# Kernel optimization log

Hardware: AMD Instinct MI355X
Metric: run time of the kernel (lower is better)

Reference implementation:

```python
import jax, jax.numpy as jnp
import numpy as np
from jax import lax

EPS = 1e-5
BETA = 0.25  # commitment cost

def _conv(x, w, b):
    y = lax.conv_general_dilated(x, w, (1, 1), 'VALID',
                                 dimension_numbers=('NCHW', 'OIHW', 'NCHW'))
    return y + b[None, :, None, None]

def _maxpool2(x):
    return lax.reduce_window(x, -jnp.inf, lax.max, (1, 1, 2, 2), (1, 1, 2, 2), 'VALID')

def _bn(x, scale, bias):
    # training-mode batch norm over (N, H, W)
    mean = jnp.mean(x, axis=(0, 2, 3), keepdims=True)
    var = jnp.var(x, axis=(0, 2, 3), keepdims=True)
    xhat = (x - mean) * lax.rsqrt(var + EPS)
    return xhat * scale[None, :, None, None] + bias[None, :, None, None]

def _vq(z_nchw, codebook):
    # z: [B,32,4,4] -> vectors [B*16, 32]
    B, C, H, W = z_nchw.shape
    z = jnp.transpose(z_nchw, (0, 2, 3, 1)).reshape(-1, C)          # [N, D]
    # squared L2 distances to codebook [K, D]
    d = (jnp.sum(z * z, axis=1, keepdims=True)
         + jnp.sum(codebook * codebook, axis=1)
         - 2.0 * z @ codebook.T)                                    # [N, K]
    idx = jnp.argmin(d, axis=1)                                     # [N]
    q = codebook[idx]                                               # [N, D]
    sg = lax.stop_gradient
    vq_loss = jnp.mean((q - sg(z)) ** 2) + BETA * jnp.mean((sg(q) - z) ** 2)
    q_st = z + sg(q - z)                                            # straight-through
    recon = jnp.transpose(q_st.reshape(B, H, W, C), (0, 3, 1, 2))
    return recon, vq_loss

def setup_inputs() -> dict:
    key = jax.random.key(0)
    ks = jax.random.split(key, 12)
    f = lambda k, shape, s: (jax.random.normal(k, shape, jnp.float32) * s)
    inp = {
        'x': jax.random.normal(ks[0], (2048, 3, 32, 32), jnp.float32),
        'conv1_w': f(ks[1], (64, 3, 3, 3), 0.1), 'conv1_b': jnp.zeros((64,), jnp.float32),
        'bn1_scale': jnp.ones((64,), jnp.float32), 'bn1_bias': jnp.zeros((64,), jnp.float32),
        'conv2_w': f(ks[2], (32, 64, 3, 3), 0.05), 'conv2_b': jnp.zeros((32,), jnp.float32),
        'bn2_scale': jnp.ones((32,), jnp.float32), 'bn2_bias': jnp.zeros((32,), jnp.float32),
        'conv3_w': f(ks[3], (32, 32, 3, 3), 0.06), 'conv3_b': jnp.zeros((32,), jnp.float32),
        'bn3_scale': jnp.ones((32,), jnp.float32), 'bn3_bias': jnp.zeros((32,), jnp.float32),
        'codebook': f(ks[4], (100, 32), 0.5),
        'fc1_w': f(ks[5], (64, 512), 0.04), 'fc1_b': jnp.zeros((64,), jnp.float32),
        'fc2_w': f(ks[6], (10, 64), 0.12), 'fc2_b': jnp.zeros((10,), jnp.float32),
    }
    return inp

def reference(x, conv1_w, conv1_b, bn1_scale, bn1_bias,
              conv2_w, conv2_b, bn2_scale, bn2_bias,
              conv3_w, conv3_b, bn3_scale, bn3_bias,
              codebook, fc1_w, fc1_b, fc2_w, fc2_b):
    h = _bn(jax.nn.relu(_maxpool2(_conv(x, conv1_w, conv1_b))), bn1_scale, bn1_bias)
    h = _bn(jax.nn.relu(_maxpool2(_conv(h, conv2_w, conv2_b))), bn2_scale, bn2_bias)
    h = _bn(jax.nn.relu(_conv(h, conv3_w, conv3_b)), bn3_scale, bn3_bias)   # [B,32,4,4]
    recon, vq_loss = _vq(h, codebook)
    blended = 0.5 * recon + h
    flat = blended.reshape(-1, 4 * 4 * 32)
    z1 = jax.nn.relu(flat @ fc1_w.T + fc1_b)
    y = z1 @ fc2_w.T + fc2_b
    return recon, h, vq_loss, jax.nn.log_softmax(y, axis=1)
```

## Files before the change

kernel.cpp:

```cpp
#include <hip/hip_runtime.h>
#include <math.h>


#define CNT1 460800.0
#define CNT2 73728.0
#define CNT3 32768.0

__global__ void k0_w2t(const float* __restrict__ w2, float* __restrict__ w2t)
{
  const int idx = blockIdx.x * 256 + threadIdx.x;
  const int o = idx & 31, q = idx >> 5;
  const int r = q % 144, cc = q / 144;
  w2t[idx] = w2[o * 576 + cc * 144 + r];
}

__global__ __launch_bounds__(256) void k1_conv1_stats(
    const float* __restrict__ x, const float* __restrict__ w1,
    const float* __restrict__ b1, double* __restrict__ dstats,
    float* __restrict__ y1, int store_y1)
{
  __shared__ float img[3072];
  __shared__ float red[512];
  const int n = blockIdx.x, t = threadIdx.x;
  const float4* xin = (const float4*)(x + n * 3072);
  float4* img4 = (float4*)img;
  for (int i = t; i < 768; i += 256) img4[i] = xin[i];
  const int c = t >> 2, q = t & 3;
  float wr[27];
#pragma unroll
  for (int k = 0; k < 27; ++k) wr[k] = w1[c * 27 + k];
  const float bias = b1[c];
  __syncthreads();
  float s = 0.f, ss = 0.f;
  for (int p = q; p < 225; p += 4) {
    const int i = p / 15, j = p % 15;
    float a0 = 0, a1 = 0, a2 = 0, a3 = 0;
#pragma unroll
    for (int cin = 0; cin < 3; ++cin) {
      float pt[4][4];
#pragma unroll
      for (int r = 0; r < 4; ++r) {
        const float2* row = (const float2*)&img[cin * 1024 + (2 * i + r) * 32 + 2 * j];
        float2 u = row[0], v = row[1];
        pt[r][0] = u.x; pt[r][1] = u.y; pt[r][2] = v.x; pt[r][3] = v.y;
      }
#pragma unroll
      for (int kh = 0; kh < 3; ++kh)
#pragma unroll
        for (int kw = 0; kw < 3; ++kw) {
          const float wv = wr[cin * 9 + kh * 3 + kw];
          a0 += pt[kh][kw] * wv;     a1 += pt[kh][kw + 1] * wv;
          a2 += pt[kh + 1][kw] * wv; a3 += pt[kh + 1][kw + 1] * wv;
        }
    }
    float v = fmaxf(fmaxf(a0, a1), fmaxf(a2, a3)) + bias;
    v = fmaxf(v, 0.f);
    if (store_y1) y1[n * 15360 + c * 240 + i * 16 + j] = v;
    s += v; ss += v * v;
  }
  red[t * 2] = s; red[t * 2 + 1] = ss;
  __syncthreads();
  if (q == 0) {
    float rs = red[t * 2] + red[(t + 1) * 2] + red[(t + 2) * 2] + red[(t + 3) * 2];
    float rq = red[t * 2 + 1] + red[(t + 1) * 2 + 1] + red[(t + 2) * 2 + 1] + red[(t + 3) * 2 + 1];
    atomicAdd(&dstats[c * 16], (double)rs);
    atomicAdd(&dstats[c * 16 + 8], (double)rq);
  }
}

__global__ void k_finalize(const double* __restrict__ dstats,
                           const float* __restrict__ scale, const float* __restrict__ bias,
                           float* __restrict__ a, float* __restrict__ b, int C, double inv_cnt)
{
  int c = threadIdx.x;
  if (c < C) {
    double mean = dstats[c * 16] * inv_cnt;
    double var = dstats[c * 16 + 8] * inv_cnt - mean * mean;
    double ai = (double)scale[c] / sqrt(var + 1e-5);
    a[c] = (float)ai;
    b[c] = (float)((double)bias[c] - mean * ai);
  }
}

__global__ __launch_bounds__(384) void k3_conv2_fast(
    const float* __restrict__ y1, const float* __restrict__ a1f,
    const float* __restrict__ b1f, const float* __restrict__ w2t,
    const float* __restrict__ b2, float* __restrict__ y2,
    double* __restrict__ dstats2)
{
  __shared__ float y1n[3840];
  __shared__ float w2c[4608];
  __shared__ float sum2L[32], ss2L[32];
  const int n = blockIdx.x, t = threadIdx.x;
  if (t < 32) { sum2L[t] = 0.f; ss2L[t] = 0.f; }
  const int co = t & 31, grp = t >> 5;
  const int irow = grp >> 1, jh = grp & 1;

  float acc[3][4];
#pragma unroll
  for (int j = 0; j < 3; ++j) { acc[j][0] = 0; acc[j][1] = 0; acc[j][2] = 0; acc[j][3] = 0; }

  for (int cc = 0; cc < 4; ++cc) {
    __syncthreads();
    {
      const float4* y1g = (const float4*)(y1 + n * 15360 + cc * 3840);
      float4* y1n4 = (float4*)y1n;
      for (int idx = t; idx < 960; idx += 384) {
        const int ci = idx / 60;
        const int ch = cc * 16 + ci;
        const float an = a1f[ch], bn = b1f[ch];
        float4 v = y1g[idx];
        v.x = an * v.x + bn; v.y = an * v.y + bn;
        v.z = an * v.z + bn; v.w = an * v.w + bn;
        y1n4[idx] = v;
      }
    }
    {
      const float4* wg = (const float4*)(w2t + cc * 4608);
      float4* wc4 = (float4*)w2c;
      for (int idx = t; idx < 1152; idx += 384) wc4[idx] = wg[idx];
    }
    __syncthreads();
    for (int ci = 0; ci < 16; ++ci) {
      float wv[9];
#pragma unroll
      for (int s = 0; s < 9; ++s) wv[s] = w2c[(ci * 9 + s) * 32 + co];
      float pt[4][8];
      const float2* base = (const float2*)&y1n[ci * 240 + (2 * irow) * 16 + 6 * jh];
#pragma unroll
      for (int r = 0; r < 4; ++r)
#pragma unroll
        for (int u = 0; u < 4; ++u) {
          float2 f = base[r * 8 + u];
          pt[r][u * 2] = f.x; pt[r][u * 2 + 1] = f.y;
        }
#pragma unroll
      for (int j = 0; j < 3; ++j)
#pragma unroll
        for (int kh = 0; kh < 3; ++kh)
#pragma unroll
          for (int kw = 0; kw < 3; ++kw) {
            const float w_ = wv[kh * 3 + kw];
            acc[j][0] += pt[kh][2 * j + kw] * w_;
            acc[j][1] += pt[kh][2 * j + 1 + kw] * w_;
            acc[j][2] += pt[kh + 1][2 * j + kw] * w_;
            acc[j][3] += pt[kh + 1][2 * j + 1 + kw] * w_;
          }
    }
  }
  {
    const float bias = b2[co];
    float s = 0.f, sq = 0.f;
#pragma unroll
    for (int j = 0; j < 3; ++j) {
      float v = fmaxf(fmaxf(acc[j][0], acc[j][1]), fmaxf(acc[j][2], acc[j][3])) + bias;
      v = fmaxf(v, 0.f);
      y2[n * 1152 + co * 36 + irow * 6 + jh * 3 + j] = v;
      s += v; sq += v * v;
    }
    atomicAdd(&sum2L[co], s);
    atomicAdd(&ss2L[co], sq);
  }
  __syncthreads();
  if (t < 32) {
    atomicAdd(&dstats2[t * 16], (double)sum2L[t]);
    atomicAdd(&dstats2[t * 16 + 8], (double)ss2L[t]);
  }
}

__global__ __launch_bounds__(256) void k3_conv2(
    const float* __restrict__ x, const float* __restrict__ w1,
    const float* __restrict__ b1, const float* __restrict__ a1f,
    const float* __restrict__ b1f, const float* __restrict__ w2,
    const float* __restrict__ b2, float* __restrict__ y2,
    double* __restrict__ dstats2)
{
  __shared__ float img[3072];
  __shared__ float y1n[16 * 240];
  __shared__ float w2c[144 * 32];
  __shared__ float sum2L[32], ss2L[32];
  const int n = blockIdx.x, t = threadIdx.x;
  if (t < 32) { sum2L[t] = 0.f; ss2L[t] = 0.f; }
  const float4* xin = (const float4*)(x + n * 3072);
  float4* img4 = (float4*)img;
  for (int i = t; i < 768; i += 256) img4[i] = xin[i];

  const int co = t & 31, irow = t >> 5;
  const bool activeC = (irow < 6);

  float acc[6][4];
#pragma unroll
  for (int j = 0; j < 6; ++j) { acc[j][0] = 0; acc[j][1] = 0; acc[j][2] = 0; acc[j][3] = 0; }

  const int cA = t >> 4, qA = t & 15;

  for (int cc = 0; cc < 4; ++cc) {
    __syncthreads();
    {
      const int ch = cc * 16 + cA;
      float wr[27];
#pragma unroll
      for (int k = 0; k < 27; ++k) wr[k] = w1[ch * 27 + k];
      const float bias = b1[ch];
      const float an = a1f[ch], bn = b1f[ch];
      for (int p = qA; p < 225; p += 16) {
        const int i = p / 15, j = p % 15;
        float a0 = 0, a1 = 0, a2 = 0, a3 = 0;
#pragma unroll
        for (int cin = 0; cin < 3; ++cin) {
          float pt[4][4];
#pragma unroll
          for (int r = 0; r < 4; ++r) {
            const float2* row = (const float2*)&img[cin * 1024 + (2 * i + r) * 32 + 2 * j];
            float2 u = row[0], v = row[1];
            pt[r][0] = u.x; pt[r][1] = u.y; pt[r][2] = v.x; pt[r][3] = v.y;
          }
#pragma unroll
          for (int kh = 0; kh < 3; ++kh)
#pragma unroll
            for (int kw = 0; kw < 3; ++kw) {
              const float wv = wr[cin * 9 + kh * 3 + kw];
              a0 += pt[kh][kw] * wv;     a1 += pt[kh][kw + 1] * wv;
              a2 += pt[kh + 1][kw] * wv; a3 += pt[kh + 1][kw + 1] * wv;
            }
        }
        float v = fmaxf(fmaxf(a0, a1), fmaxf(a2, a3)) + bias;
        v = fmaxf(v, 0.f);
        y1n[cA * 240 + i * 16 + j] = an * v + bn;
      }
    }
    for (int idx = t; idx < 4608; idx += 256) {
      const int o = idx & 31, r = idx >> 5;
      w2c[r * 32 + o] = w2[o * 576 + cc * 144 + r];
    }
    __syncthreads();
    if (activeC) {
      for (int ci = 0; ci < 16; ++ci) {
        float wv[9];
#pragma unroll
        for (int s = 0; s < 9; ++s) wv[s] = w2c[(ci * 9 + s) * 32 + co];
        float pt[4][16];
        const float4* src = (const float4*)&y1n[ci * 240 + (2 * irow) * 16];
#pragma unroll
        for (int r = 0; r < 4; ++r)
#pragma unroll
          for (int u = 0; u < 4; ++u) {
            float4 f = src[r * 4 + u];
            pt[r][u * 4] = f.x; pt[r][u * 4 + 1] = f.y;
            pt[r][u * 4 + 2] = f.z; pt[r][u * 4 + 3] = f.w;
          }
#pragma unroll
        for (int j = 0; j < 6; ++j) {
#pragma unroll
          for (int kh = 0; kh < 3; ++kh)
#pragma unroll
            for (int kw = 0; kw < 3; ++kw) {
              const float w_ = wv[kh * 3 + kw];
              acc[j][0] += pt[kh][2 * j + kw] * w_;
              acc[j][1] += pt[kh][2 * j + 1 + kw] * w_;
              acc[j][2] += pt[kh + 1][2 * j + kw] * w_;
              acc[j][3] += pt[kh + 1][2 * j + 1 + kw] * w_;
            }
        }
      }
    }
  }
  if (activeC) {
    const float bias = b2[co];
    float s = 0.f, sq = 0.f;
#pragma unroll
    for (int j = 0; j < 6; ++j) {
      float v = fmaxf(fmaxf(acc[j][0], acc[j][1]), fmaxf(acc[j][2], acc[j][3])) + bias;
      v = fmaxf(v, 0.f);
      y2[n * 1152 + co * 36 + irow * 6 + j] = v;
      s += v; sq += v * v;
    }
    atomicAdd(&sum2L[co], s);
    atomicAdd(&ss2L[co], sq);
  }
  __syncthreads();
  if (t < 32) {
    atomicAdd(&dstats2[t * 16], (double)sum2L[t]);
    atomicAdd(&dstats2[t * 16 + 8], (double)ss2L[t]);
  }
}

__global__ __launch_bounds__(256) void k5_conv3(
    const float* __restrict__ y2, const float* __restrict__ a2f,
    const float* __restrict__ b2f, const float* __restrict__ w3,
    const float* __restrict__ b3, float* __restrict__ t3,
    double* __restrict__ dstats3)
{
  __shared__ float y2n[8 * 1152];
  __shared__ float w3c[32 * 144];
  __shared__ float sum3L[32], ss3L[32];
  const int blk = blockIdx.x, t = threadIdx.x;
  if (t < 32) { sum3L[t] = 0.f; ss3L[t] = 0.f; }
  for (int idx = t; idx < 9216; idx += 256) {
    const int ci = (idx % 1152) / 36;
    y2n[idx] = a2f[ci] * y2[blk * 9216 + idx] + b2f[ci];
  }
  const int il = t >> 5, c = t & 31;
  float acc[16];
#pragma unroll
  for (int p = 0; p < 16; ++p) acc[p] = 0.f;
  for (int ch = 0; ch < 2; ++ch) {
    __syncthreads();
    for (int idx = t; idx < 4608; idx += 256) {
      int o = idx / 144, r = idx % 144;
      w3c[idx] = w3[o * 288 + ch * 144 + r];
    }
    __syncthreads();
    for (int ci = 0; ci < 16; ++ci) {
      float wv[9];
#pragma unroll
      for (int s = 0; s < 9; ++s) wv[s] = w3c[c * 144 + ci * 9 + s];
      float pt[36];
      const float4* src = (const float4*)&y2n[il * 1152 + (ch * 16 + ci) * 36];
#pragma unroll
      for (int u = 0; u < 9; ++u) {
        float4 f = src[u];
        pt[u * 4] = f.x; pt[u * 4 + 1] = f.y; pt[u * 4 + 2] = f.z; pt[u * 4 + 3] = f.w;
      }
#pragma unroll
      for (int i = 0; i < 4; ++i)
#pragma unroll
        for (int j = 0; j < 4; ++j) {
          float a_ = 0.f;
#pragma unroll
          for (int kh = 0; kh < 3; ++kh)
#pragma unroll
            for (int kw = 0; kw < 3; ++kw)
              a_ += pt[(i + kh) * 6 + j + kw] * wv[kh * 3 + kw];
          acc[i * 4 + j] += a_;
        }
    }
  }
  const float bias = b3[c];
  float s = 0.f, sq = 0.f;
  float vout[16];
#pragma unroll
  for (int p = 0; p < 16; ++p) {
    float v = fmaxf(acc[p] + bias, 0.f);
    vout[p] = v; s += v; sq += v * v;
  }
  const int n = blk * 8 + il;
  float4* dst = (float4*)&t3[(n * 32 + c) * 16];
#pragma unroll
  for (int u = 0; u < 4; ++u)
    dst[u] = make_float4(vout[u * 4], vout[u * 4 + 1], vout[u * 4 + 2], vout[u * 4 + 3]);
  atomicAdd(&sum3L[c], s);
  atomicAdd(&ss3L[c], sq);
  __syncthreads();
  if (t < 32) {
    atomicAdd(&dstats3[t * 16], (double)sum3L[t]);
    atomicAdd(&dstats3[t * 16 + 8], (double)ss3L[t]);
  }
}

__global__ __launch_bounds__(256) void k7_h(
    const float* __restrict__ t3, const float* __restrict__ a3,
    const float* __restrict__ b3, float* __restrict__ hout)
{
  const int idx = blockIdx.x * 256 + threadIdx.x;
  float4 v = ((const float4*)t3)[idx];
  const int c = (idx >> 2) & 31;
  const float a = a3[c], b = b3[c];
  float4 o;
  o.x = a * v.x + b; o.y = a * v.y + b; o.z = a * v.z + b; o.w = a * v.w + b;
  ((float4*)hout)[idx] = o;
}

__global__ __launch_bounds__(256) void k8_vq(
    const float* __restrict__ h, const float* __restrict__ cbg,
    float* __restrict__ recon, double* __restrict__ dloss)
{
  __shared__ float cb[3200];
  __shared__ float n2[100];
  const int t = threadIdx.x;
  for (int i = t; i < 3200; i += 256) cb[i] = cbg[i];
  __syncthreads();
  if (t < 100) {
    float s = 0.f;
#pragma unroll
    for (int c = 0; c < 32; ++c) { float v = cb[t * 32 + c]; s += v * v; }
    n2[t] = s;
  }
  __syncthreads();
  const int v = blockIdx.x * 256 + t;
  const int b = v >> 4, p = v & 15;
  float z[32];
  float z2 = 0.f;
#pragma unroll
  for (int c = 0; c < 32; ++c) {
    float zz = h[b * 512 + c * 16 + p];
    z[c] = zz; z2 += zz * zz;
  }
  float best = 1e30f; int bi = 0;
  for (int k = 0; k < 100; ++k) {
    float dot = 0.f;
#pragma unroll
    for (int c = 0; c < 32; ++c) dot += z[c] * cb[k * 32 + c];
    const float d = z2 + n2[k] - 2.f * dot;
    if (d < best) { best = d; bi = k; }
  }
  float lsum = 0.f;
#pragma unroll
  for (int c = 0; c < 32; ++c) {
    const float qv = cb[bi * 32 + c];
    recon[b * 512 + c * 16 + p] = qv;
    const float df = qv - z[c];
    lsum += df * df;
  }
#pragma unroll
  for (int off = 32; off > 0; off >>= 1) lsum += __shfl_down(lsum, off, 64);
  if ((t & 63) == 0) atomicAdd(dloss, (double)lsum);
}

__global__ void k9_loss(const double* __restrict__ dloss, float* __restrict__ out)
{
  out[0] = (float)(1.25 * dloss[0] / (32768.0 * 32.0));
}

__global__ __launch_bounds__(256) void k10_fc(
    const float* __restrict__ recon, const float* __restrict__ h,
    const float* __restrict__ fc1w, const float* __restrict__ fc1b,
    const float* __restrict__ fc2w, const float* __restrict__ fc2b,
    float* __restrict__ out)
{
  __shared__ float flat[4 * 512];
  __shared__ float z1[4 * 64];
  __shared__ float yL[4 * 10];
  const int t = threadIdx.x;
  const int w = t >> 6, l = t & 63;
  const int n = blockIdx.x * 4 + w;
  for (int k = l; k < 512; k += 64)
    flat[w * 512 + k] = 0.5f * recon[n * 512 + k] + h[n * 512 + k];
  __syncthreads();
  float acc = fc1b[l];
  const float4* wrow = (const float4*)(fc1w + l * 512);
  const float4* frow = (const float4*)(flat + w * 512);
  for (int k4 = 0; k4 < 128; ++k4) {
    const float4 wv = wrow[k4], fv = frow[k4];
    acc += wv.x * fv.x + wv.y * fv.y + wv.z * fv.z + wv.w * fv.w;
  }
  z1[w * 64 + l] = fmaxf(acc, 0.f);
  __syncthreads();
  if (l < 10) {
    float a = fc2b[l];
#pragma unroll
    for (int i = 0; i < 64; ++i) a += fc2w[l * 64 + i] * z1[w * 64 + i];
    yL[w * 10 + l] = a;
  }
  __syncthreads();
  if (l < 10) {
    float m = -1e30f;
#pragma unroll
    for (int i = 0; i < 10; ++i) m = fmaxf(m, yL[w * 10 + i]);
    float s = 0.f;
#pragma unroll
    for (int i = 0; i < 10; ++i) s += expf(yL[w * 10 + i] - m);
    out[n * 10 + l] = yL[w * 10 + l] - m - logf(s);
  }
}

extern "C" void kernel_launch(void* const* d_in, const int* in_sizes, int n_in,
                              void* d_out, int out_size, void* d_ws, size_t ws_size,
                              hipStream_t stream)
{
  (void)in_sizes; (void)n_in; (void)out_size;
  const float* x    = (const float*)d_in[0];
  const float* w1   = (const float*)d_in[1];
  const float* cb1  = (const float*)d_in[2];
  const float* bn1s = (const float*)d_in[3];
  const float* bn1b = (const float*)d_in[4];
  const float* w2   = (const float*)d_in[5];
  const float* cb2  = (const float*)d_in[6];
  const float* bn2s = (const float*)d_in[7];
  const float* bn2b = (const float*)d_in[8];
  const float* w3   = (const float*)d_in[9];
  const float* cb3  = (const float*)d_in[10];
  const float* bn3s = (const float*)d_in[11];
  const float* bn3b = (const float*)d_in[12];
  const float* cbk  = (const float*)d_in[13];
  const float* fc1w = (const float*)d_in[14];
  const float* fc1b = (const float*)d_in[15];
  const float* fc2w = (const float*)d_in[16];
  const float* fc2b = (const float*)d_in[17];
  float* out = (float*)d_out;

  double* dstats = (double*)d_ws;
  float* fws = (float*)((char*)d_ws + 32768);
  float* a1 = fws;        float* b1 = fws + 64;
  float* a2 = fws + 128;  float* b2 = fws + 160;
  float* a3 = fws + 192;  float* b3 = fws + 224;

  float* recon_out = out;
  float* h_out     = out + 1048576;
  float* loss_out  = out + 2097152;
  float* y_out     = out + 2097153;

  const bool fast = ws_size >= 139568128ull;

  hipMemsetAsync(d_ws, 0, 32768, stream);

  if (fast) {
    float* w2t = fws + 256;
    float* y2  = fws + 256 + 18432;
    float* t3  = y2 + 2359296;
    float* y1  = t3 + 1048576;

    k0_w2t<<<72, 256, 0, stream>>>(w2, w2t);
    k1_conv1_stats<<<2048, 256, 0, stream>>>(x, w1, cb1, dstats, y1, 1);
    k_finalize<<<1, 64, 0, stream>>>(dstats, bn1s, bn1b, a1, b1, 64, 1.0 / CNT1);
    k3_conv2_fast<<<2048, 384, 0, stream>>>(y1, a1, b1, w2t, cb2, y2, dstats + 1024);
    k_finalize<<<1, 64, 0, stream>>>(dstats + 1024, bn2s, bn2b, a2, b2, 32, 1.0 / CNT2);
    k5_conv3<<<256, 256, 0, stream>>>(y2, a2, b2, w3, cb3, t3, dstats + 1536);
    k_finalize<<<1, 64, 0, stream>>>(dstats + 1536, bn3s, bn3b, a3, b3, 32, 1.0 / CNT3);
    k7_h<<<1024, 256, 0, stream>>>(t3, a3, b3, h_out);
    k8_vq<<<128, 256, 0, stream>>>(h_out, cbk, recon_out, dstats + 2048);
    k9_loss<<<1, 1, 0, stream>>>(dstats + 2048, loss_out);
    k10_fc<<<512, 256, 0, stream>>>(recon_out, h_out, fc1w, fc1b, fc2w, fc2b, y_out);
  } else {
    float* y2 = fws + 256;
    float* t3 = fws + 256 + 2359296;

    k1_conv1_stats<<<2048, 256, 0, stream>>>(x, w1, cb1, dstats, nullptr, 0);
    k_finalize<<<1, 64, 0, stream>>>(dstats, bn1s, bn1b, a1, b1, 64, 1.0 / CNT1);
    k3_conv2<<<2048, 256, 0, stream>>>(x, w1, cb1, a1, b1, w2, cb2, y2, dstats + 1024);
    k_finalize<<<1, 64, 0, stream>>>(dstats + 1024, bn2s, bn2b, a2, b2, 32, 1.0 / CNT2);
    k5_conv3<<<256, 256, 0, stream>>>(y2, a2, b2, w3, cb3, t3, dstats + 1536);
    k_finalize<<<1, 64, 0, stream>>>(dstats + 1536, bn3s, bn3b, a3, b3, 32, 1.0 / CNT3);
    k7_h<<<1024, 256, 0, stream>>>(t3, a3, b3, h_out);
    k8_vq<<<128, 256, 0, stream>>>(h_out, cbk, recon_out, dstats + 2048);
    k9_loss<<<1, 1, 0, stream>>>(dstats + 2048, loss_out);
    k10_fc<<<512, 256, 0, stream>>>(recon_out, h_out, fc1w, fc1b, fc2w, fc2b, y_out);
  }
}
```

Baseline: 537.0 us.

## Retile conv1/conv2 kernels for register reuse and fuse small tail kernels

Conv1 is rewritten so each thread computes a full pooled row for one channel, using float4 loads and vectorized stores. Conv2 now processes four images per block, with each thread producing two output channels across six pooled columns, and the weights are repacked to match. The BN3 apply is folded into the VQ kernel and the loss write into the FC kernel, removing two launches. The cost is higher register pressure from larger per-thread accumulator tiles and a different shared-memory layout.

```diff
diff --git a/kernel.cpp b/kernel.cpp
--- a/kernel.cpp
+++ b/kernel.cpp
@@ -9,15 +9,97 @@
 __global__ void k0_w2t(const float* __restrict__ w2, float* __restrict__ w2t)
 {
   const int idx = blockIdx.x * 256 + threadIdx.x;
-  const int o = idx & 31, q = idx >> 5;
-  const int r = q % 144, cc = q / 144;
-  w2t[idx] = w2[o * 576 + cc * 144 + r];
+  const int half = idx & 1, cog = (idx >> 1) & 15;
+  const int r = (idx >> 5) % 72, cc = idx / 2304;
+  const int o = cog + 16 * half;
+  w2t[idx] = w2[o * 576 + cc * 72 + r];
+}
+
+template<int CB, int W4, int J0, int CNT>
+__device__ __forceinline__ void conv1_seg(const float* img, const float* wr,
+                                          int prow, float bias, float* vout)
+{
+  float acc[CNT][4];
+#pragma unroll
+  for (int j = 0; j < CNT; ++j) { acc[j][0] = 0; acc[j][1] = 0; acc[j][2] = 0; acc[j][3] = 0; }
+#pragma unroll
+  for (int cin = 0; cin < 3; ++cin) {
+    float pt[4][4 * W4];
+    const float4* src = (const float4*)&img[cin * 1024 + (2 * prow) * 32 + CB];
+#pragma unroll
+    for (int r = 0; r < 4; ++r)
+#pragma unroll
+      for (int u = 0; u < W4; ++u) {
+        float4 f = src[r * 8 + u];
+        pt[r][u * 4 + 0] = f.x; pt[r][u * 4 + 1] = f.y;
+        pt[r][u * 4 + 2] = f.z; pt[r][u * 4 + 3] = f.w;
+      }
+#pragma unroll
+    for (int jj = 0; jj < CNT; ++jj) {
+      const int c0 = 2 * (J0 + jj) - CB;
+#pragma unroll
+      for (int kh = 0; kh < 3; ++kh)
+#pragma unroll
+        for (int kw = 0; kw < 3; ++kw) {
+          const float w_ = wr[cin * 9 + kh * 3 + kw];
+          acc[jj][0] += pt[kh][c0 + kw] * w_;
+          acc[jj][1] += pt[kh][c0 + 1 + kw] * w_;
+          acc[jj][2] += pt[kh + 1][c0 + kw] * w_;
+          acc[jj][3] += pt[kh + 1][c0 + 1 + kw] * w_;
+        }
+    }
+  }
+#pragma unroll
+  for (int jj = 0; jj < CNT; ++jj) {
+    float v = fmaxf(fmaxf(acc[jj][0], acc[jj][1]), fmaxf(acc[jj][2], acc[jj][3])) + bias;
+    vout[J0 + jj] = fmaxf(v, 0.f);
+  }
+}
+
+__global__ __launch_bounds__(256) void k1_conv1(
+    const float* __restrict__ x, const float* __restrict__ w1,
+    const float* __restrict__ b1, double* __restrict__ dstats,
+    float* __restrict__ y1)
+{
+  __shared__ float img[3072];
+  __shared__ float red_s[256], red_q[256];
+  const int n = blockIdx.x, t = threadIdx.x;
+  const float4* xin = (const float4*)(x + n * 3072);
+  float4* img4 = (float4*)img;
+  for (int i = t; i < 768; i += 256) img4[i] = xin[i];
+  const int ch = t & 63, rslot = t >> 6;
+  float wr[27];
+#pragma unroll
+  for (int k = 0; k < 27; ++k) wr[k] = w1[ch * 27 + k];
+  const float bias = b1[ch];
+  __syncthreads();
+  float s = 0.f, ss = 0.f;
+  for (int prow = rslot; prow < 15; prow += 4) {
+    float vout[15];
+    conv1_seg<0, 4, 0, 7>(img, wr, prow, bias, vout);
+    conv1_seg<12, 4, 7, 5>(img, wr, prow, bias, vout);
+    conv1_seg<24, 2, 12, 3>(img, wr, prow, bias, vout);
+    float4* dst = (float4*)(y1 + n * 15360 + ch * 240 + prow * 16);
+    dst[0] = make_float4(vout[0], vout[1], vout[2], vout[3]);
+    dst[1] = make_float4(vout[4], vout[5], vout[6], vout[7]);
+    dst[2] = make_float4(vout[8], vout[9], vout[10], vout[11]);
+    dst[3] = make_float4(vout[12], vout[13], vout[14], 0.f);
+#pragma unroll
+    for (int j = 0; j < 15; ++j) { s += vout[j]; ss += vout[j] * vout[j]; }
+  }
+  red_s[t] = s; red_q[t] = ss;
+  __syncthreads();
+  if (t < 64) {
+    float rs = red_s[t] + red_s[t + 64] + red_s[t + 128] + red_s[t + 192];
+    float rq = red_q[t] + red_q[t + 64] + red_q[t + 128] + red_q[t + 192];
+    atomicAdd(&dstats[t * 16], (double)rs);
+    atomicAdd(&dstats[t * 16 + 8], (double)rq);
+  }
 }
 
 __global__ __launch_bounds__(256) void k1_conv1_stats(
     const float* __restrict__ x, const float* __restrict__ w1,
-    const float* __restrict__ b1, double* __restrict__ dstats,
-    float* __restrict__ y1, int store_y1)
+    const float* __restrict__ b1, double* __restrict__ dstats)
 {
   __shared__ float img[3072];
   __shared__ float red[512];
@@ -55,7 +137,6 @@
     }
     float v = fmaxf(fmaxf(a0, a1), fmaxf(a2, a3)) + bias;
     v = fmaxf(v, 0.f);
-    if (store_y1) y1[n * 15360 + c * 240 + i * 16 + j] = v;
     s += v; ss += v * v;
   }
   red[t * 2] = s; red[t * 2 + 1] = ss;
@@ -88,74 +169,81 @@
     const float* __restrict__ b2, float* __restrict__ y2,
     double* __restrict__ dstats2)
 {
-  __shared__ float y1n[3840];
-  __shared__ float w2c[4608];
+  __shared__ float y1n[4 * 1928];
+  __shared__ float w2c[72 * 32];
   __shared__ float sum2L[32], ss2L[32];
-  const int n = blockIdx.x, t = threadIdx.x;
+  const int t = threadIdx.x;
+  const int n0 = blockIdx.x * 4;
   if (t < 32) { sum2L[t] = 0.f; ss2L[t] = 0.f; }
-  const int co = t & 31, grp = t >> 5;
-  const int irow = grp >> 1, jh = grp & 1;
-
-  float acc[3][4];
-#pragma unroll
-  for (int j = 0; j < 3; ++j) { acc[j][0] = 0; acc[j][1] = 0; acc[j][2] = 0; acc[j][3] = 0; }
-
-  for (int cc = 0; cc < 4; ++cc) {
+  const int irow = t / 64;
+  const int img = (t >> 4) & 3;
+  const int cog = t & 15;
+
+  float acc[2][6][4];
+#pragma unroll
+  for (int h = 0; h < 2; ++h)
+#pragma unroll
+    for (int j = 0; j < 6; ++j) { acc[h][j][0] = 0; acc[h][j][1] = 0; acc[h][j][2] = 0; acc[h][j][3] = 0; }
+
+  for (int cc = 0; cc < 8; ++cc) {
     __syncthreads();
-    {
-      const float4* y1g = (const float4*)(y1 + n * 15360 + cc * 3840);
-      float4* y1n4 = (float4*)y1n;
-      for (int idx = t; idx < 960; idx += 384) {
-        const int ci = idx / 60;
-        const int ch = cc * 16 + ci;
-        const float an = a1f[ch], bn = b1f[ch];
-        float4 v = y1g[idx];
-        v.x = an * v.x + bn; v.y = an * v.y + bn;
-        v.z = an * v.z + bn; v.w = an * v.w + bn;
-        y1n4[idx] = v;
+    for (int idx = t; idx < 1920; idx += 384) {
+      const int im = idx / 480, wi = idx - im * 480;
+      const int ch = cc * 8 + wi / 60;
+      const float an = a1f[ch], bn = b1f[ch];
+      float4 v = ((const float4*)(y1 + (n0 + im) * 15360 + cc * 1920))[wi];
+      v.x = an * v.x + bn; v.y = an * v.y + bn;
+      v.z = an * v.z + bn; v.w = an * v.w + bn;
+      ((float4*)y1n)[im * 482 + wi] = v;
+    }
+    for (int idx = t; idx < 576; idx += 384)
+      ((float4*)w2c)[idx] = ((const float4*)(w2t + cc * 2304))[idx];
+    __syncthreads();
+    for (int ci = 0; ci < 8; ++ci) {
+      float wv0[9], wv1[9];
+#pragma unroll
+      for (int s = 0; s < 9; ++s) {
+        float2 wp = *(const float2*)&w2c[(ci * 9 + s) * 32 + cog * 2];
+        wv0[s] = wp.x; wv1[s] = wp.y;
       }
-    }
-    {
-      const float4* wg = (const float4*)(w2t + cc * 4608);
-      float4* wc4 = (float4*)w2c;
-      for (int idx = t; idx < 1152; idx += 384) wc4[idx] = wg[idx];
-    }
-    __syncthreads();
-    for (int ci = 0; ci < 16; ++ci) {
-      float wv[9];
-#pragma unroll
-      for (int s = 0; s < 9; ++s) wv[s] = w2c[(ci * 9 + s) * 32 + co];
-      float pt[4][8];
-      const float2* base = (const float2*)&y1n[ci * 240 + (2 * irow) * 16 + 6 * jh];
+      float pt[4][16];
+      const float4* src = (const float4*)&y1n[img * 1928 + ci * 240 + 2 * irow * 16];
 #pragma unroll
       for (int r = 0; r < 4; ++r)
 #pragma unroll
         for (int u = 0; u < 4; ++u) {
-          float2 f = base[r * 8 + u];
-          pt[r][u * 2] = f.x; pt[r][u * 2 + 1] = f.y;
+          float4 f = src[r * 4 + u];
+          pt[r][u * 4 + 0] = f.x; pt[r][u * 4 + 1] = f.y;
+          pt[r][u * 4 + 2] = f.z; pt[r][u * 4 + 3] = f.w;
         }
 #pragma unroll
-      for (int j = 0; j < 3; ++j)
+      for (int j = 0; j < 6; ++j)
 #pragma unroll
         for (int kh = 0; kh < 3; ++kh)
 #pragma unroll
           for (int kw = 0; kw < 3; ++kw) {
-            const float w_ = wv[kh * 3 + kw];
-            acc[j][0] += pt[kh][2 * j + kw] * w_;
-            acc[j][1] += pt[kh][2 * j + 1 + kw] * w_;
-            acc[j][2] += pt[kh + 1][2 * j + kw] * w_;
-            acc[j][3] += pt[kh + 1][2 * j + 1 + kw] * w_;
+            const float p00 = pt[kh][2 * j + kw],     p01 = pt[kh][2 * j + 1 + kw];
+            const float p10 = pt[kh + 1][2 * j + kw], p11 = pt[kh + 1][2 * j + 1 + kw];
+            const float w0 = wv0[kh * 3 + kw], w1_ = wv1[kh * 3 + kw];
+            acc[0][j][0] += p00 * w0;  acc[0][j][1] += p01 * w0;
+            acc[0][j][2] += p10 * w0;  acc[0][j][3] += p11 * w0;
+            acc[1][j][0] += p00 * w1_; acc[1][j][1] += p01 * w1_;
+            acc[1][j][2] += p10 * w1_; acc[1][j][3] += p11 * w1_;
           }
     }
   }
-  {
+  const int n = n0 + img;
+#pragma unroll
+  for (int half = 0; half < 2; ++half) {
+    const int co = cog + half * 16;
     const float bias = b2[co];
     float s = 0.f, sq = 0.f;
 #pragma unroll
-    for (int j = 0; j < 3; ++j) {
-      float v = fmaxf(fmaxf(acc[j][0], acc[j][1]), fmaxf(acc[j][2], acc[j][3])) + bias;
+    for (int j = 0; j < 6; ++j) {
+      float v = fmaxf(fmaxf(acc[half][j][0], acc[half][j][1]),
+                      fmaxf(acc[half][j][2], acc[half][j][3])) + bias;
       v = fmaxf(v, 0.f);
-      y2[n * 1152 + co * 36 + irow * 6 + jh * 3 + j] = v;
+      y2[n * 1152 + co * 36 + irow * 6 + j] = v;
       s += v; sq += v * v;
     }
     atomicAdd(&sum2L[co], s);
@@ -358,22 +446,11 @@
   }
 }
 
-__global__ __launch_bounds__(256) void k7_h(
-    const float* __restrict__ t3, const float* __restrict__ a3,
-    const float* __restrict__ b3, float* __restrict__ hout)
-{
-  const int idx = blockIdx.x * 256 + threadIdx.x;
-  float4 v = ((const float4*)t3)[idx];
-  const int c = (idx >> 2) & 31;
-  const float a = a3[c], b = b3[c];
-  float4 o;
-  o.x = a * v.x + b; o.y = a * v.y + b; o.z = a * v.z + b; o.w = a * v.w + b;
-  ((float4*)hout)[idx] = o;
-}
-
 __global__ __launch_bounds__(256) void k8_vq(
-    const float* __restrict__ h, const float* __restrict__ cbg,
-    float* __restrict__ recon, double* __restrict__ dloss)
+    const float* __restrict__ t3, const float* __restrict__ a3f,
+    const float* __restrict__ b3f, const float* __restrict__ cbg,
+    float* __restrict__ recon, float* __restrict__ hout,
+    double* __restrict__ dloss)
 {
   __shared__ float cb[3200];
   __shared__ float n2[100];
@@ -393,7 +470,8 @@
   float z2 = 0.f;
 #pragma unroll
   for (int c = 0; c < 32; ++c) {
-    float zz = h[b * 512 + c * 16 + p];
+    const float zz = a3f[c] * t3[b * 512 + c * 16 + p] + b3f[c];
+    hout[b * 512 + c * 16 + p] = zz;
     z[c] = zz; z2 += zz * zz;
   }
   float best = 1e30f; int bi = 0;
@@ -417,16 +495,12 @@
   if ((t & 63) == 0) atomicAdd(dloss, (double)lsum);
 }
 
-__global__ void k9_loss(const double* __restrict__ dloss, float* __restrict__ out)
-{
-  out[0] = (float)(1.25 * dloss[0] / (32768.0 * 32.0));
-}
-
 __global__ __launch_bounds__(256) void k10_fc(
     const float* __restrict__ recon, const float* __restrict__ h,
     const float* __restrict__ fc1w, const float* __restrict__ fc1b,
     const float* __restrict__ fc2w, const float* __restrict__ fc2b,
-    float* __restrict__ out)
+    float* __restrict__ out, const double* __restrict__ dloss,
+    float* __restrict__ loss_out)
 {
   __shared__ float flat[4 * 512];
   __shared__ float z1[4 * 64];
@@ -434,6 +508,8 @@
   const int t = threadIdx.x;
   const int w = t >> 6, l = t & 63;
   const int n = blockIdx.x * 4 + w;
+  if (blockIdx.x == 0 && t == 0)
+    loss_out[0] = (float)(1.25 * dloss[0] / (32768.0 * 32.0));
   for (int k = l; k < 512; k += 64)
     flat[w * 512 + k] = 0.5f * recon[n * 512 + k] + h[n * 512 + k];
   __syncthreads();
@@ -511,29 +587,27 @@
     float* y1  = t3 + 1048576;
 
     k0_w2t<<<72, 256, 0, stream>>>(w2, w2t);
-    k1_conv1_stats<<<2048, 256, 0, stream>>>(x, w1, cb1, dstats, y1, 1);
+    k1_conv1<<<2048, 256, 0, stream>>>(x, w1, cb1, dstats, y1);
     k_finalize<<<1, 64, 0, stream>>>(dstats, bn1s, bn1b, a1, b1, 64, 1.0 / CNT1);
-    k3_conv2_fast<<<2048, 384, 0, stream>>>(y1, a1, b1, w2t, cb2, y2, dstats + 1024);
+    k3_conv2_fast<<<512, 384, 0, stream>>>(y1, a1, b1, w2t, cb2, y2, dstats + 1024);
     k_finalize<<<1, 64, 0, stream>>>(dstats + 1024, bn2s, bn2b, a2, b2, 32, 1.0 / CNT2);
     k5_conv3<<<256, 256, 0, stream>>>(y2, a2, b2, w3, cb3, t3, dstats + 1536);
     k_finalize<<<1, 64, 0, stream>>>(dstats + 1536, bn3s, bn3b, a3, b3, 32, 1.0 / CNT3);
-    k7_h<<<1024, 256, 0, stream>>>(t3, a3, b3, h_out);
-    k8_vq<<<128, 256, 0, stream>>>(h_out, cbk, recon_out, dstats + 2048);
-    k9_loss<<<1, 1, 0, stream>>>(dstats + 2048, loss_out);
-    k10_fc<<<512, 256, 0, stream>>>(recon_out, h_out, fc1w, fc1b, fc2w, fc2b, y_out);
+    k8_vq<<<128, 256, 0, stream>>>(t3, a3, b3, cbk, recon_out, h_out, dstats + 2048);
+    k10_fc<<<512, 256, 0, stream>>>(recon_out, h_out, fc1w, fc1b, fc2w, fc2b,
+                                    y_out, dstats + 2048, loss_out);
   } else {
     float* y2 = fws + 256;
     float* t3 = fws + 256 + 2359296;
 
-    k1_conv1_stats<<<2048, 256, 0, stream>>>(x, w1, cb1, dstats, nullptr, 0);
+    k1_conv1_stats<<<2048, 256, 0, stream>>>(x, w1, cb1, dstats);
     k_finalize<<<1, 64, 0, stream>>>(dstats, bn1s, bn1b, a1, b1, 64, 1.0 / CNT1);
     k3_conv2<<<2048, 256, 0, stream>>>(x, w1, cb1, a1, b1, w2, cb2, y2, dstats + 1024);
     k_finalize<<<1, 64, 0, stream>>>(dstats + 1024, bn2s, bn2b, a2, b2, 32, 1.0 / CNT2);
     k5_conv3<<<256, 256, 0, stream>>>(y2, a2, b2, w3, cb3, t3, dstats + 1536);
     k_finalize<<<1, 64, 0, stream>>>(dstats + 1536, bn3s, bn3b, a3, b3, 32, 1.0 / CNT3);
-    k7_h<<<1024, 256, 0, stream>>>(t3, a3, b3, h_out);
-    k8_vq<<<128, 256, 0, stream>>>(h_out, cbk, recon_out, dstats + 2048);
-    k9_loss<<<1, 1, 0, stream>>>(dstats + 2048, loss_out);
-    k10_fc<<<512, 256, 0, stream>>>(recon_out, h_out, fc1w, fc1b, fc2w, fc2b, y_out);
-  }
-}
+    k8_vq<<<128, 256, 0, stream>>>(t3, a3, b3, cbk, recon_out, h_out, dstats + 2048);
+    k10_fc<<<512, 256, 0, stream>>>(recon_out, h_out, fc1w, fc1b, fc2w, fc2b,
+                                    y_out, dstats + 2048, loss_out);
+  }
+}
```

Result: faster. 463.4 us (-13.7%).
